# Optimization experiments

Hardware: AMD Instinct MI355X
Metric: run time of the kernel (lower is better)

Reference implementation:

```python
import jax, jax.numpy as jnp
import numpy as np

# Module constants (from init_kwargs)
ANCHORS = np.array([[116.0, 90.0], [156.0, 198.0], [373.0, 326.0]], dtype=np.float32)
ANCHOR_AREAS = jnp.asarray(ANCHORS[:, 0] * ANCHORS[:, 1])  # [A]
A, H, W, C = 3, 128, 128, 2
IMG_W, IMG_H = 1024.0, 1024.0
STRIDE_W, STRIDE_H = IMG_W / H, IMG_H / W
ATTRS = 5 + C
LAMBDA_XY, LAMBDA_WH, LAMBDA_CONF, LAMBDA_CLS = 2.5, 2.5, 1.0, 1.0


def setup_inputs() -> dict:
    key = jax.random.key(0)
    k1, k2, k3, k4, k5 = jax.random.split(key, 5)
    B, T = 64, 2
    # conf/class feed BCELoss -> predictions must lie in [0,1)
    output = jax.random.uniform(k1, (B, A * H * W * ATTRS), dtype=jnp.float32)
    # Corner-format target boxes constructed so the (buggy) cell index
    # int((w - cx)/stride) is always within [0, mapSize).
    x1 = jax.random.uniform(k2, (B, T), minval=0.0, maxval=20.0)
    y1 = jax.random.uniform(k3, (B, T), minval=0.0, maxval=20.0)
    x2 = x1 + jax.random.uniform(k4, (B, T), minval=200.0, maxval=880.0)
    y2 = y1 + jax.random.uniform(k5, (B, T), minval=200.0, maxval=880.0)
    boxes = jnp.stack([x1, y1, x2, y2], axis=-1)  # [B,T,4]
    areas = (x2 - x1) * (y2 - y1)                 # [B,T]
    labels = jnp.ones((B, T), dtype=jnp.int32)    # label 1 -> valid for both one-hot quirks
    return {"output": output, "boxes": boxes, "labels": labels, "areas": areas}


def _bce(p, t):
    # torch BCELoss: mean, with log clamped to -100
    lp = jnp.maximum(jnp.log(p), -100.0)
    l1p = jnp.maximum(jnp.log1p(-p), -100.0)
    return -jnp.mean(t * lp + (1.0 - t) * l1p)


def _mse(p, t):
    return jnp.mean((p - t) ** 2)


def yolo_loss(output, boxes, labels, areas):
    B = output.shape[0]
    T = boxes.shape[1]
    out = output.reshape(B, A, H, W, ATTRS)
    x, y, w, h, conf = out[..., 0], out[..., 1], out[..., 2], out[..., 3], out[..., 4]
    cls = out[..., 5:]  # [B,A,H,W,C]

    gx = jnp.arange(H, dtype=output.dtype)[None, None, :, None]  # xCoord axis
    gy = jnp.arange(W, dtype=output.dtype)[None, None, None, :]  # yCoord axis
    x = x - gx
    y = y - gy

    # convert target boxes corners -> center format (done in-place in the original)
    cx = (boxes[..., 0] + boxes[..., 2]) * 0.5
    cy = (boxes[..., 1] + boxes[..., 3]) * 0.5
    bw = boxes[..., 2] - boxes[..., 0]
    bh = boxes[..., 3] - boxes[..., 1]
    tb = jnp.stack([cx, cy, bw, bh], axis=-1)  # [B,T,4]

    # class one-hots: target 0 uses labels[0]; targets i>=1 use labels[i]-1 (original quirk)
    cls0 = jax.nn.one_hot(labels[:, 0], C, dtype=output.dtype)
    cls1 = jax.nn.one_hot(labels[:, 1] - 1, C, dtype=output.dtype)
    tcls = jnp.stack([cls0, cls1], axis=1)            # [B,T,C]
    full = jnp.concatenate([tb, tcls], axis=-1)       # [B,T,4+C]

    best_anchor = jnp.argmin(jnp.abs(ANCHOR_AREAS[None, None, :] - areas[..., None]), axis=-1)  # [B,T]
    # original computes cell as int((w - cx)/stride), int((h - cy)/stride)
    cellX = ((bw - cx) / STRIDE_W).astype(jnp.int32)
    cellY = ((bh - cy) / STRIDE_H).astype(jnp.int32)

    mask = jnp.zeros((B, A, H, W), jnp.int32)
    exact = jnp.zeros((B, A, H, W), bool)
    bidx = jnp.arange(B)
    for i in range(T):  # tiny fixed loop over targets; later targets overwrite, as in torch
        mask = mask.at[bidx, best_anchor[:, i], cellX[:, i], cellY[:, i]].set(i)
        exact = exact.at[bidx, best_anchor[:, i], cellX[:, i], cellY[:, i]].set(True)

    matched = full[bidx[:, None, None, None], mask]  # [B,A,H,W,4+C]

    zero = jnp.zeros((), output.dtype)
    tX = jnp.where(exact, matched[..., 0] - gx, zero)
    tY = jnp.where(exact, matched[..., 1] - gy, zero)
    tW = jnp.where(exact, matched[..., 2], zero)
    tH = jnp.where(exact, matched[..., 3], zero)
    tConf = exact.astype(output.dtype)
    # targetMatched[5:] has length C-1==1 and broadcasts to all C slots (original quirk)
    tCls = jnp.where(exact[..., None], jnp.broadcast_to(matched[..., 5:6], cls.shape), zero)

    # IOU: prediction (x-gx, y-gy, w, h) converted center->corners; target center-format
    # boxes are (incorrectly, but faithfully) treated as corners.
    px1, py1 = x - w * 0.5, y - h * 0.5
    px2, py2 = x + w * 0.5, y + h * 0.5
    tx1 = tb[..., 0][:, None, None, None, :]  # [B,1,1,1,T]
    ty1 = tb[..., 1][:, None, None, None, :]
    tx2 = tb[..., 2][:, None, None, None, :]
    ty2 = tb[..., 3][:, None, None, None, :]
    ix = jnp.clip(jnp.minimum(px2[..., None], tx2) - jnp.maximum(px1[..., None], tx1), 0.0)
    iy = jnp.clip(jnp.minimum(py2[..., None], ty2) - jnp.maximum(py1[..., None], ty1), 0.0)
    inter = ix * iy                                   # [B,A,H,W,T]
    area_p = (px2 - px1) * (py2 - py1)                # [B,A,H,W]
    area_t = ((tx2 - tx1) * (ty2 - ty1))              # [B,1,1,1,T]
    iou = inter / (area_p[..., None] + area_t - inter + 1e-16)
    max_iou = jnp.max(iou, axis=-1)                   # [B,A,H,W]

    suppress = jnp.logical_and(~exact, max_iou > 0.5)
    xf = jnp.where(exact, x, zero)
    yf = jnp.where(exact, y, zero)
    wf = jnp.where(exact, w, zero)
    hf = jnp.where(exact, h, zero)
    clsf = jnp.where(exact[..., None], cls, zero)
    conff = jnp.where(suppress, zero, conf)

    xL, yL = _mse(xf, tX), _mse(yf, tY)
    wL, hL = _mse(wf, tW), _mse(hf, tH)
    confL = _bce(conff, tConf)
    clsL = _bce(clsf, tCls)
    loss = (xL + yL) * LAMBDA_XY + (wL + hL) * LAMBDA_WH + confL * LAMBDA_CONF + clsL * LAMBDA_CLS
    return (loss, xL, yL, wL, hL, confL, clsL)


def reference(output, boxes, labels, areas):
    return yolo_loss(output, boxes, labels, areas)
```

## Files before the change

kernel.cpp:

```cpp
#include <hip/hip_runtime.h>
#include <math.h>

#define A_ 3
#define H_ 128
#define W_ 128
#define C_ 2
#define ATTRS 7
#define B_ 64
#define CELLS_PER_BATCH (A_*H_*W_)
#define TOTAL_CELLS (B_*CELLS_PER_BATCH)

#define NBLK 1536
#define NTHR 256
#define ITERS (TOTAL_CELLS / (NBLK*NTHR))
#define NSLOTS 32

__global__ __launch_bounds__(192) void zero_ws_k(float* ws) {
    ws[threadIdx.x] = 0.0f;
}

__global__ __launch_bounds__(NTHR) void yolo_main_k(
    const float* __restrict__ outp,
    const float* __restrict__ boxes,
    const int*   __restrict__ labels,
    const float* __restrict__ areas,
    float* __restrict__ ws)
{
    __shared__ float4 s_tile[448];
    __shared__ float  s_red[4][6];
    const int tid = threadIdx.x;

    float accX = 0.f, accY = 0.f, accW = 0.f, accH = 0.f, accC = 0.f, accK = 0.f;

    for (int it = 0; it < ITERS; ++it) {
        const int base = (blockIdx.x + it * NBLK) * NTHR;
        if (it) __syncthreads();
        const float4* gp = (const float4*)(outp + (size_t)base * ATTRS);
        s_tile[tid] = gp[tid];
        if (tid < 192) s_tile[tid + 256] = gp[tid + 256];
        __syncthreads();

        const int b     = base / CELLS_PER_BATCH;
        const int rbase = base - b * CELLS_PER_BATCH;

        float cxA[2], cyA[2], bwA[2], bhA[2], atA[2], t5A[2];
        int   baA[2], cXA[2], cYA[2];
        #pragma unroll
        for (int t = 0; t < 2; ++t) {
            const float x1 = boxes[b*8 + t*4 + 0];
            const float y1 = boxes[b*8 + t*4 + 1];
            const float x2 = boxes[b*8 + t*4 + 2];
            const float y2 = boxes[b*8 + t*4 + 3];
            const float cx = (x1 + x2) * 0.5f, cy = (y1 + y2) * 0.5f;
            const float bw = x2 - x1,          bh = y2 - y1;
            cxA[t] = cx; cyA[t] = cy; bwA[t] = bw; bhA[t] = bh;
            atA[t] = (bw - cx) * (bh - cy);
            const float ar = areas[b*2 + t];
            const float d0 = fabsf(10440.f - ar);
            const float d1 = fabsf(30888.f - ar);
            const float d2 = fabsf(121598.f - ar);
            int ba = 0; float bd = d0;
            if (d1 < bd) { ba = 1; bd = d1; }
            if (d2 < bd) { ba = 2; }
            baA[t] = ba;
            cXA[t] = (int)((bw - cx) * 0.125f);
            cYA[t] = (int)((bh - cy) * 0.125f);
            const int lab = labels[b*2 + t];
            t5A[t] = (t == 0) ? (lab == 1 ? 1.f : 0.f) : (lab == 2 ? 1.f : 0.f);
        }

        const int r = rbase + tid;
        const int a = r >> 14;
        const int i = (r >> 7) & 127;
        const int j = r & 127;
        const float* sp = ((const float*)s_tile) + tid * ATTRS;
        const float xr = sp[0], yr = sp[1], w = sp[2], h = sp[3];
        const float conf = sp[4], c0 = sp[5], c1 = sp[6];

        const float fi = (float)i, fj = (float)j;
        const float x = xr - fi, y = yr - fj;
        const float hw = 0.5f * w, hh = 0.5f * h;
        const float px1 = x - hw, px2 = x + hw;
        const float py1 = y - hh, py2 = y + hh;
        const float areaP = (px2 - px1) * (py2 - py1);

        bool e[2]; float iou[2];
        #pragma unroll
        for (int t = 0; t < 2; ++t) {
            e[t] = (a == baA[t]) && (i == cXA[t]) && (j == cYA[t]);
            const float ix = fmaxf(fminf(px2, bwA[t]) - fmaxf(px1, cxA[t]), 0.f);
            const float iy = fmaxf(fminf(py2, bhA[t]) - fmaxf(py1, cyA[t]), 0.f);
            const float in_ = ix * iy;
            iou[t] = in_ / (areaP + atA[t] - in_ + 1e-16f);
        }
        const bool  exact = e[0] || e[1];
        const float miou  = fmaxf(iou[0], iou[1]);
        const bool  suppress = (!exact) && (miou > 0.5f);

        if (exact) {
            const int t = e[1] ? 1 : 0;
            const float dx = x - (cxA[t] - fi); accX += dx * dx;
            const float dy = y - (cyA[t] - fj); accY += dy * dy;
            const float dw = w - bwA[t];        accW += dw * dw;
            const float dh = h - bhA[t];        accH += dh * dh;
            accC += fmaxf(logf(conf), -100.f);
            if (t5A[t] != 0.f)
                accK += fmaxf(logf(c0), -100.f) + fmaxf(logf(c1), -100.f);
            else
                accK += fmaxf(log1pf(-c0), -100.f) + fmaxf(log1pf(-c1), -100.f);
        } else if (!suppress) {
            accC += fmaxf(log1pf(-conf), -100.f);
        }
    }

    float v[6] = {accX, accY, accW, accH, accC, accK};
    #pragma unroll
    for (int m = 0; m < 6; ++m) {
        float s = v[m];
        #pragma unroll
        for (int off = 32; off > 0; off >>= 1) s += __shfl_down(s, off, 64);
        v[m] = s;
    }
    const int wid = tid >> 6;
    if ((tid & 63) == 0) {
        #pragma unroll
        for (int m = 0; m < 6; ++m) s_red[wid][m] = v[m];
    }
    __syncthreads();
    if (tid < 6) {
        const float s = s_red[0][tid] + s_red[1][tid] + s_red[2][tid] + s_red[3][tid];
        atomicAdd(&ws[(blockIdx.x & (NSLOTS - 1)) * 6 + tid], s);
    }
}

__global__ __launch_bounds__(64) void finalize_k(const float* __restrict__ ws,
                                                 float* __restrict__ o)
{
    if (threadIdx.x == 0) {
        float s0=0,s1=0,s2=0,s3=0,s4=0,s5=0;
        for (int k = 0; k < NSLOTS; ++k) {
            s0 += ws[k*6+0]; s1 += ws[k*6+1]; s2 += ws[k*6+2];
            s3 += ws[k*6+3]; s4 += ws[k*6+4]; s5 += ws[k*6+5];
        }
        const float N = (float)TOTAL_CELLS;
        const float xL = s0 / N, yL = s1 / N, wL = s2 / N, hL = s3 / N;
        const float confL = -s4 / N;
        const float clsL  = -s5 / (N * (float)C_);
        o[0] = 2.5f * (xL + yL) + 2.5f * (wL + hL) + confL + clsL;
        o[1] = xL; o[2] = yL; o[3] = wL; o[4] = hL; o[5] = confL; o[6] = clsL;
    }
}

extern "C" void kernel_launch(void* const* d_in, const int* in_sizes, int n_in,
                              void* d_out, int out_size, void* d_ws, size_t ws_size,
                              hipStream_t stream) {
    const float* outp   = (const float*)d_in[0];
    const float* boxes  = (const float*)d_in[1];
    const int*   labels = (const int*)d_in[2];
    const float* areas  = (const float*)d_in[3];
    float* ws = (float*)d_ws;
    float* o  = (float*)d_out;

    zero_ws_k<<<1, 192, 0, stream>>>(ws);
    yolo_main_k<<<NBLK, NTHR, 0, stream>>>(outp, boxes, labels, areas, ws);
    finalize_k<<<1, 64, 0, stream>>>(ws, o);
}
```

Before: 139.8 us.

## Precompute per-batch box data and fuse finalize into main kernel via last-block reduction

A prep kernel now zeroes the workspace and computes each batch's target-box parameters once, including a flat cell code, in place of the per-iteration recomputation done in every block. Each main-kernel block now handles a contiguous run of cells within a single batch and loads the precomputed parameters once. The exact-cell test becomes a single index compare. The separate finalize launch is replaced by a last-block-done atomic counter that performs the final reduction inside the main kernel. This saves one launch and redundant scalar work, at the cost of a threadfence and counter atomic in every block.

```diff
diff --git a/kernel.cpp b/kernel.cpp
--- a/kernel.cpp
+++ b/kernel.cpp
@@ -12,39 +12,25 @@
 
 #define NBLK 1536
 #define NTHR 256
-#define ITERS (TOTAL_CELLS / (NBLK*NTHR))
+#define CELLS_PER_BLK (TOTAL_CELLS/NBLK)
+#define BLKS_PER_BATCH (CELLS_PER_BATCH/CELLS_PER_BLK)
+#define ITERS (CELLS_PER_BLK/NTHR)
 #define NSLOTS 32
 
-__global__ __launch_bounds__(192) void zero_ws_k(float* ws) {
-    ws[threadIdx.x] = 0.0f;
-}
+#define WS_CNT   200
+#define WS_BATCH 256
 
-__global__ __launch_bounds__(NTHR) void yolo_main_k(
-    const float* __restrict__ outp,
+__global__ __launch_bounds__(256) void prep_k(
     const float* __restrict__ boxes,
     const int*   __restrict__ labels,
     const float* __restrict__ areas,
     float* __restrict__ ws)
 {
-    __shared__ float4 s_tile[448];
-    __shared__ float  s_red[4][6];
     const int tid = threadIdx.x;
-
-    float accX = 0.f, accY = 0.f, accW = 0.f, accH = 0.f, accC = 0.f, accK = 0.f;
-
-    for (int it = 0; it < ITERS; ++it) {
-        const int base = (blockIdx.x + it * NBLK) * NTHR;
-        if (it) __syncthreads();
-        const float4* gp = (const float4*)(outp + (size_t)base * ATTRS);
-        s_tile[tid] = gp[tid];
-        if (tid < 192) s_tile[tid + 256] = gp[tid + 256];
-        __syncthreads();
-
-        const int b     = base / CELLS_PER_BATCH;
-        const int rbase = base - b * CELLS_PER_BATCH;
-
-        float cxA[2], cyA[2], bwA[2], bhA[2], atA[2], t5A[2];
-        int   baA[2], cXA[2], cYA[2];
+    ws[tid] = 0.0f;
+    if (tid < B_) {
+        const int b = tid;
+        float o16[16];
         #pragma unroll
         for (int t = 0; t < 2; ++t) {
             const float x1 = boxes[b*8 + t*4 + 0];
@@ -53,8 +39,7 @@
             const float y2 = boxes[b*8 + t*4 + 3];
             const float cx = (x1 + x2) * 0.5f, cy = (y1 + y2) * 0.5f;
             const float bw = x2 - x1,          bh = y2 - y1;
-            cxA[t] = cx; cyA[t] = cy; bwA[t] = bw; bhA[t] = bh;
-            atA[t] = (bw - cx) * (bh - cy);
+            const float at = (bw - cx) * (bh - cy);
             const float ar = areas[b*2 + t];
             const float d0 = fabsf(10440.f - ar);
             const float d1 = fabsf(30888.f - ar);
@@ -62,15 +47,49 @@
             int ba = 0; float bd = d0;
             if (d1 < bd) { ba = 1; bd = d1; }
             if (d2 < bd) { ba = 2; }
-            baA[t] = ba;
-            cXA[t] = (int)((bw - cx) * 0.125f);
-            cYA[t] = (int)((bh - cy) * 0.125f);
+            const int cX = (int)((bw - cx) * 0.125f);
+            const int cY = (int)((bh - cy) * 0.125f);
+            const int code = ba * (H_*W_) + cX * W_ + cY;
             const int lab = labels[b*2 + t];
-            t5A[t] = (t == 0) ? (lab == 1 ? 1.f : 0.f) : (lab == 2 ? 1.f : 0.f);
+            const float t5 = (t == 0) ? (lab == 1 ? 1.f : 0.f)
+                                      : (lab == 2 ? 1.f : 0.f);
+            o16[t*8+0]=cx; o16[t*8+1]=cy; o16[t*8+2]=bw; o16[t*8+3]=bh;
+            o16[t*8+4]=at; o16[t*8+5]=t5; o16[t*8+6]=(float)code; o16[t*8+7]=0.f;
         }
+        #pragma unroll
+        for (int k = 0; k < 16; ++k) ws[WS_BATCH + b*16 + k] = o16[k];
+    }
+}
 
-        const int r = rbase + tid;
-        const int a = r >> 14;
+__global__ __launch_bounds__(NTHR) void yolo_main_k(
+    const float* __restrict__ outp,
+    float* __restrict__ ws,
+    float* __restrict__ o)
+{
+    __shared__ float4 s_tile[448];
+    __shared__ float  s_red[4][6];
+    __shared__ int    s_last;
+    __shared__ float  s_out[6];
+    const int tid = threadIdx.x;
+
+    const int b       = blockIdx.x / BLKS_PER_BATCH;
+    const int colBase = (blockIdx.x % BLKS_PER_BATCH) * CELLS_PER_BLK;
+    const float4* wsb = (const float4*)(ws + WS_BATCH) + b*4;
+    const float4 p0 = wsb[0], q0 = wsb[1];
+    const float4 p1 = wsb[2], q1 = wsb[3];
+    const int code0 = (int)q0.z, code1 = (int)q1.z;
+
+    float accX = 0.f, accY = 0.f, accW = 0.f, accH = 0.f, accC = 0.f, accK = 0.f;
+
+    for (int it = 0; it < ITERS; ++it) {
+        const int base = blockIdx.x * CELLS_PER_BLK + it * NTHR;
+        if (it) __syncthreads();
+        const float4* gp = (const float4*)(outp + (size_t)base * ATTRS);
+        s_tile[tid] = gp[tid];
+        if (tid < 192) s_tile[tid + 256] = gp[tid + 256];
+        __syncthreads();
+
+        const int r = colBase + it * NTHR + tid;
         const int i = (r >> 7) & 127;
         const int j = r & 127;
         const float* sp = ((const float*)s_tile) + tid * ATTRS;
@@ -84,27 +103,29 @@
         const float py1 = y - hh, py2 = y + hh;
         const float areaP = (px2 - px1) * (py2 - py1);
 
-        bool e[2]; float iou[2];
-        #pragma unroll
-        for (int t = 0; t < 2; ++t) {
-            e[t] = (a == baA[t]) && (i == cXA[t]) && (j == cYA[t]);
-            const float ix = fmaxf(fminf(px2, bwA[t]) - fmaxf(px1, cxA[t]), 0.f);
-            const float iy = fmaxf(fminf(py2, bhA[t]) - fmaxf(py1, cyA[t]), 0.f);
-            const float in_ = ix * iy;
-            iou[t] = in_ / (areaP + atA[t] - in_ + 1e-16f);
-        }
-        const bool  exact = e[0] || e[1];
-        const float miou  = fmaxf(iou[0], iou[1]);
-        const bool  suppress = (!exact) && (miou > 0.5f);
+        const float ix0 = fmaxf(fminf(px2, p0.z) - fmaxf(px1, p0.x), 0.f);
+        const float iy0 = fmaxf(fminf(py2, p0.w) - fmaxf(py1, p0.y), 0.f);
+        const float in0 = ix0 * iy0;
+        const float iou0 = in0 / (areaP + q0.x - in0 + 1e-16f);
+        const float ix1 = fmaxf(fminf(px2, p1.z) - fmaxf(px1, p1.x), 0.f);
+        const float iy1 = fmaxf(fminf(py2, p1.w) - fmaxf(py1, p1.y), 0.f);
+        const float in1 = ix1 * iy1;
+        const float iou1 = in1 / (areaP + q1.x - in1 + 1e-16f);
+
+        const bool e0 = (r == code0), e1 = (r == code1);
+        const bool exact = e0 || e1;
+        const bool suppress = (!exact) && (fmaxf(iou0, iou1) > 0.5f);
 
         if (exact) {
-            const int t = e[1] ? 1 : 0;
-            const float dx = x - (cxA[t] - fi); accX += dx * dx;
-            const float dy = y - (cyA[t] - fj); accY += dy * dy;
-            const float dw = w - bwA[t];        accW += dw * dw;
-            const float dh = h - bhA[t];        accH += dh * dh;
+            const float cx = e1 ? p1.x : p0.x, cy = e1 ? p1.y : p0.y;
+            const float bw = e1 ? p1.z : p0.z, bh = e1 ? p1.w : p0.w;
+            const float t5 = e1 ? q1.y : q0.y;
+            const float dx = x - (cx - fi); accX += dx * dx;
+            const float dy = y - (cy - fj); accY += dy * dy;
+            const float dw = w - bw;        accW += dw * dw;
+            const float dh = h - bh;        accH += dh * dh;
             accC += fmaxf(logf(conf), -100.f);
-            if (t5A[t] != 0.f)
+            if (t5 != 0.f)
                 accK += fmaxf(logf(c0), -100.f) + fmaxf(logf(c1), -100.f);
             else
                 accK += fmaxf(log1pf(-c0), -100.f) + fmaxf(log1pf(-c1), -100.f);
@@ -129,23 +150,28 @@
     __syncthreads();
     if (tid < 6) {
         const float s = s_red[0][tid] + s_red[1][tid] + s_red[2][tid] + s_red[3][tid];
-        atomicAdd(&ws[(blockIdx.x & (NSLOTS - 1)) * 6 + tid], s);
+        atomicAdd(&ws[tid * NSLOTS + (blockIdx.x & (NSLOTS - 1))], s);
     }
-}
 
-__global__ __launch_bounds__(64) void finalize_k(const float* __restrict__ ws,
-                                                 float* __restrict__ o)
-{
-    if (threadIdx.x == 0) {
-        float s0=0,s1=0,s2=0,s3=0,s4=0,s5=0;
-        for (int k = 0; k < NSLOTS; ++k) {
-            s0 += ws[k*6+0]; s1 += ws[k*6+1]; s2 += ws[k*6+2];
-            s3 += ws[k*6+3]; s4 += ws[k*6+4]; s5 += ws[k*6+5];
-        }
+    if (tid == 0) {
+        __threadfence();
+        const unsigned old = atomicAdd((unsigned*)(ws + WS_CNT), 1u);
+        s_last = (old == NBLK - 1u);
+    }
+    __syncthreads();
+    if (!s_last) return;
+
+    float s = (tid < 6 * NSLOTS) ? atomicAdd(&ws[tid], 0.0f) : 0.f;
+    #pragma unroll
+    for (int off = 16; off > 0; off >>= 1) s += __shfl_xor(s, off, 64);
+    if (tid < 6 * NSLOTS && (tid & 31) == 0) s_out[tid >> 5] = s;
+    __syncthreads();
+    if (tid == 0) {
         const float N = (float)TOTAL_CELLS;
-        const float xL = s0 / N, yL = s1 / N, wL = s2 / N, hL = s3 / N;
-        const float confL = -s4 / N;
-        const float clsL  = -s5 / (N * (float)C_);
+        const float xL = s_out[0] / N, yL = s_out[1] / N;
+        const float wL = s_out[2] / N, hL = s_out[3] / N;
+        const float confL = -s_out[4] / N;
+        const float clsL  = -s_out[5] / (N * (float)C_);
         o[0] = 2.5f * (xL + yL) + 2.5f * (wL + hL) + confL + clsL;
         o[1] = xL; o[2] = yL; o[3] = wL; o[4] = hL; o[5] = confL; o[6] = clsL;
     }
@@ -161,7 +187,6 @@
     float* ws = (float*)d_ws;
     float* o  = (float*)d_out;
 
-    zero_ws_k<<<1, 192, 0, stream>>>(ws);
-    yolo_main_k<<<NBLK, NTHR, 0, stream>>>(outp, boxes, labels, areas, ws);
-    finalize_k<<<1, 64, 0, stream>>>(ws, o);
+    prep_k<<<1, NTHR, 0, stream>>>(boxes, labels, areas, ws);
+    yolo_main_k<<<NBLK, NTHR, 0, stream>>>(outp, ws, o);
 }
```

New measurement: 185.1 us. 32.4% more time.

## Restructure main kernel to load 1024 cells per block up front

Applied to the files above, without the earlier changes.

Each block now covers 1024 contiguous cells within a single batch. It issues seven float4 loads per thread into registers up front, then does one shared-memory store and one barrier, instead of looping with a sync on every iteration. Box preprocessing is hoisted out and done once per block, the exact-cell test collapses to one packed index compare, and the IoU division becomes a multiply-compare. Logs use the fast __logf, and finalize uses a transposed workspace with a wavefront shuffle reduction. The fast log and the 1-x form reduce accuracy near 0 and 1, and the larger shared tile may lower occupancy.

```diff
diff --git a/kernel.cpp b/kernel.cpp
--- a/kernel.cpp
+++ b/kernel.cpp
@@ -10,9 +10,10 @@
 #define CELLS_PER_BATCH (A_*H_*W_)
 #define TOTAL_CELLS (B_*CELLS_PER_BATCH)
 
-#define NBLK 1536
+#define NBLK 3072
 #define NTHR 256
-#define ITERS (TOTAL_CELLS / (NBLK*NTHR))
+#define CELLS_PER_BLK 1024
+#define BLKS_PER_BATCH 48
 #define NSLOTS 32
 
 __global__ __launch_bounds__(192) void zero_ws_k(float* ws) {
@@ -26,100 +27,98 @@
     const float* __restrict__ areas,
     float* __restrict__ ws)
 {
-    __shared__ float4 s_tile[448];
+    __shared__ float4 s_tile[1792];
     __shared__ float  s_red[4][6];
     const int tid = threadIdx.x;
 
-    float accX = 0.f, accY = 0.f, accW = 0.f, accH = 0.f, accC = 0.f, accK = 0.f;
+    const float4* gp = (const float4*)outp + (size_t)blockIdx.x * 1792;
+    float4 L0 = gp[tid], L1 = gp[tid+256], L2 = gp[tid+512], L3 = gp[tid+768];
+    float4 L4 = gp[tid+1024], L5 = gp[tid+1280], L6 = gp[tid+1536];
 
-    for (int it = 0; it < ITERS; ++it) {
-        const int base = (blockIdx.x + it * NBLK) * NTHR;
-        if (it) __syncthreads();
-        const float4* gp = (const float4*)(outp + (size_t)base * ATTRS);
-        s_tile[tid] = gp[tid];
-        if (tid < 192) s_tile[tid + 256] = gp[tid + 256];
-        __syncthreads();
+    const int b  = blockIdx.x / BLKS_PER_BATCH;
+    const int r0 = (blockIdx.x % BLKS_PER_BATCH) * CELLS_PER_BLK;
+    float cxA[2], cyA[2], bwA[2], bhA[2], atA[2], t5A[2]; int codeA[2];
+    #pragma unroll
+    for (int t = 0; t < 2; ++t) {
+        const float x1 = boxes[b*8 + t*4 + 0];
+        const float y1 = boxes[b*8 + t*4 + 1];
+        const float x2 = boxes[b*8 + t*4 + 2];
+        const float y2 = boxes[b*8 + t*4 + 3];
+        const float cx = (x1 + x2) * 0.5f, cy = (y1 + y2) * 0.5f;
+        const float bw = x2 - x1,          bh = y2 - y1;
+        cxA[t]=cx; cyA[t]=cy; bwA[t]=bw; bhA[t]=bh;
+        atA[t] = (bw - cx) * (bh - cy);
+        const float ar = areas[b*2 + t];
+        const float d0 = fabsf(10440.f - ar);
+        const float d1 = fabsf(30888.f - ar);
+        const float d2 = fabsf(121598.f - ar);
+        int ba = 0; float bd = d0;
+        if (d1 < bd) { ba = 1; bd = d1; }
+        if (d2 < bd) { ba = 2; }
+        const int cX = (int)((bw - cx) * 0.125f);
+        const int cY = (int)((bh - cy) * 0.125f);
+        codeA[t] = ba * (H_*W_) + cX * W_ + cY;
+        const int lab = labels[b*2 + t];
+        t5A[t] = (t == 0) ? (lab == 1 ? 1.f : 0.f) : (lab == 2 ? 1.f : 0.f);
+    }
 
-        const int b     = base / CELLS_PER_BATCH;
-        const int rbase = base - b * CELLS_PER_BATCH;
+    s_tile[tid]      = L0; s_tile[tid+256]  = L1; s_tile[tid+512]  = L2;
+    s_tile[tid+768]  = L3; s_tile[tid+1024] = L4; s_tile[tid+1280] = L5;
+    s_tile[tid+1536] = L6;
+    __syncthreads();
 
-        float cxA[2], cyA[2], bwA[2], bhA[2], atA[2], t5A[2];
-        int   baA[2], cXA[2], cYA[2];
-        #pragma unroll
-        for (int t = 0; t < 2; ++t) {
-            const float x1 = boxes[b*8 + t*4 + 0];
-            const float y1 = boxes[b*8 + t*4 + 1];
-            const float x2 = boxes[b*8 + t*4 + 2];
-            const float y2 = boxes[b*8 + t*4 + 3];
-            const float cx = (x1 + x2) * 0.5f, cy = (y1 + y2) * 0.5f;
-            const float bw = x2 - x1,          bh = y2 - y1;
-            cxA[t] = cx; cyA[t] = cy; bwA[t] = bw; bhA[t] = bh;
-            atA[t] = (bw - cx) * (bh - cy);
-            const float ar = areas[b*2 + t];
-            const float d0 = fabsf(10440.f - ar);
-            const float d1 = fabsf(30888.f - ar);
-            const float d2 = fabsf(121598.f - ar);
-            int ba = 0; float bd = d0;
-            if (d1 < bd) { ba = 1; bd = d1; }
-            if (d2 < bd) { ba = 2; }
-            baA[t] = ba;
-            cXA[t] = (int)((bw - cx) * 0.125f);
-            cYA[t] = (int)((bh - cy) * 0.125f);
-            const int lab = labels[b*2 + t];
-            t5A[t] = (t == 0) ? (lab == 1 ? 1.f : 0.f) : (lab == 2 ? 1.f : 0.f);
-        }
+    float accX=0.f, accY=0.f, accW=0.f, accH=0.f, accC=0.f, accK=0.f;
 
-        const int r = rbase + tid;
-        const int a = r >> 14;
-        const int i = (r >> 7) & 127;
-        const int j = r & 127;
-        const float* sp = ((const float*)s_tile) + tid * ATTRS;
+    #pragma unroll
+    for (int g = 0; g < 4; ++g) {
+        const int c = tid + 256*g;
+        const int r = r0 + c;
+        const float* sp = ((const float*)s_tile) + c*ATTRS;
         const float xr = sp[0], yr = sp[1], w = sp[2], h = sp[3];
         const float conf = sp[4], c0 = sp[5], c1 = sp[6];
 
-        const float fi = (float)i, fj = (float)j;
+        const float fi = (float)((r >> 7) & 127);
+        const float fj = (float)(r & 127);
         const float x = xr - fi, y = yr - fj;
-        const float hw = 0.5f * w, hh = 0.5f * h;
+        const float hw = 0.5f*w, hh = 0.5f*h;
         const float px1 = x - hw, px2 = x + hw;
         const float py1 = y - hh, py2 = y + hh;
-        const float areaP = (px2 - px1) * (py2 - py1);
+        const float areaP = w * h;
 
-        bool e[2]; float iou[2];
-        #pragma unroll
-        for (int t = 0; t < 2; ++t) {
-            e[t] = (a == baA[t]) && (i == cXA[t]) && (j == cYA[t]);
-            const float ix = fmaxf(fminf(px2, bwA[t]) - fmaxf(px1, cxA[t]), 0.f);
-            const float iy = fmaxf(fminf(py2, bhA[t]) - fmaxf(py1, cyA[t]), 0.f);
-            const float in_ = ix * iy;
-            iou[t] = in_ / (areaP + atA[t] - in_ + 1e-16f);
-        }
-        const bool  exact = e[0] || e[1];
-        const float miou  = fmaxf(iou[0], iou[1]);
-        const bool  suppress = (!exact) && (miou > 0.5f);
+        const float ix0 = fmaxf(fminf(px2, bwA[0]) - fmaxf(px1, cxA[0]), 0.f);
+        const float iy0 = fmaxf(fminf(py2, bhA[0]) - fmaxf(py1, cyA[0]), 0.f);
+        const float in0 = ix0 * iy0;
+        const float ix1 = fmaxf(fminf(px2, bwA[1]) - fmaxf(px1, cxA[1]), 0.f);
+        const float iy1 = fmaxf(fminf(py2, bhA[1]) - fmaxf(py1, cyA[1]), 0.f);
+        const float in1 = ix1 * iy1;
+
+        const bool e0 = (r == codeA[0]), e1 = (r == codeA[1]);
+        const bool exact = e0 || e1;
+        const bool sup = (!exact) &&
+            ((3.f*in0 > areaP + atA[0]) || (3.f*in1 > areaP + atA[1]));
 
         if (exact) {
-            const int t = e[1] ? 1 : 0;
+            const int t = e1 ? 1 : 0;
             const float dx = x - (cxA[t] - fi); accX += dx * dx;
             const float dy = y - (cyA[t] - fj); accY += dy * dy;
             const float dw = w - bwA[t];        accW += dw * dw;
             const float dh = h - bhA[t];        accH += dh * dh;
-            accC += fmaxf(logf(conf), -100.f);
+            accC += fmaxf(__logf(conf), -100.f);
             if (t5A[t] != 0.f)
-                accK += fmaxf(logf(c0), -100.f) + fmaxf(logf(c1), -100.f);
+                accK += fmaxf(__logf(c0), -100.f) + fmaxf(__logf(c1), -100.f);
             else
-                accK += fmaxf(log1pf(-c0), -100.f) + fmaxf(log1pf(-c1), -100.f);
-        } else if (!suppress) {
-            accC += fmaxf(log1pf(-conf), -100.f);
+                accK += fmaxf(__logf(1.f - c0), -100.f)
+                      + fmaxf(__logf(1.f - c1), -100.f);
+        } else if (!sup) {
+            accC += fmaxf(__logf(1.f - conf), -100.f);
         }
     }
 
     float v[6] = {accX, accY, accW, accH, accC, accK};
     #pragma unroll
     for (int m = 0; m < 6; ++m) {
-        float s = v[m];
         #pragma unroll
-        for (int off = 32; off > 0; off >>= 1) s += __shfl_down(s, off, 64);
-        v[m] = s;
+        for (int off = 32; off > 0; off >>= 1) v[m] += __shfl_down(v[m], off, 64);
     }
     const int wid = tid >> 6;
     if ((tid & 63) == 0) {
@@ -129,23 +128,32 @@
     __syncthreads();
     if (tid < 6) {
         const float s = s_red[0][tid] + s_red[1][tid] + s_red[2][tid] + s_red[3][tid];
-        atomicAdd(&ws[(blockIdx.x & (NSLOTS - 1)) * 6 + tid], s);
+        atomicAdd(&ws[tid * NSLOTS + (blockIdx.x & (NSLOTS - 1))], s);
     }
 }
 
 __global__ __launch_bounds__(64) void finalize_k(const float* __restrict__ ws,
                                                  float* __restrict__ o)
 {
-    if (threadIdx.x == 0) {
-        float s0=0,s1=0,s2=0,s3=0,s4=0,s5=0;
-        for (int k = 0; k < NSLOTS; ++k) {
-            s0 += ws[k*6+0]; s1 += ws[k*6+1]; s2 += ws[k*6+2];
-            s3 += ws[k*6+3]; s4 += ws[k*6+4]; s5 += ws[k*6+5];
-        }
+    const int lane = threadIdx.x & 63;
+    float sa = ws[lane];
+    float sb = ws[64 + lane];
+    float sc = ws[128 + lane];
+    #pragma unroll
+    for (int off = 16; off > 0; off >>= 1) {
+        sa += __shfl_xor(sa, off, 64);
+        sb += __shfl_xor(sb, off, 64);
+        sc += __shfl_xor(sc, off, 64);
+    }
+    const float m1 = __shfl(sa, 32, 64);
+    const float m3 = __shfl(sb, 32, 64);
+    const float m5 = __shfl(sc, 32, 64);
+    if (lane == 0) {
         const float N = (float)TOTAL_CELLS;
-        const float xL = s0 / N, yL = s1 / N, wL = s2 / N, hL = s3 / N;
-        const float confL = -s4 / N;
-        const float clsL  = -s5 / (N * (float)C_);
+        const float xL = sa / N, yL = m1 / N;
+        const float wL = sb / N, hL = m3 / N;
+        const float confL = -sc / N;
+        const float clsL  = -m5 / (N * (float)C_);
         o[0] = 2.5f * (xL + yL) + 2.5f * (wL + hL) + confL + clsL;
         o[1] = xL; o[2] = yL; o[3] = wL; o[4] = hL; o[5] = confL; o[6] = clsL;
     }
```

After: 150.9 us. 8.0% more time.
